# Optimization experiments

Hardware: AMD Instinct MI355X
Metric: run time of the kernel (lower is better)

The kernel has to match this reference:

```python
import jax, jax.numpy as jnp
import numpy as np

EPS = 1e-5
NEG_SLOPE = 0.01  # nn.LeakyReLU default


def _layer_norm(x, scale, bias):
    mu = jnp.mean(x, axis=-1, keepdims=True)
    var = jnp.mean(jnp.square(x - mu), axis=-1, keepdims=True)
    return (x - mu) * jax.lax.rsqrt(var + EPS) * scale + bias


def _graph_conv(x, W, b, edge_src, edge_dst, dinv_out, dinv_in, n_nodes):
    # DGL GraphConv, norm='both': rst = LeakyReLU( (D_in^{-1/2} A D_out^{-1/2} x) W + b )
    h = x * dinv_out[:, None]
    agg = jax.ops.segment_sum(h[edge_src], edge_dst, num_segments=n_nodes)
    rst = agg * dinv_in[:, None]
    return jax.nn.leaky_relu(rst @ W + b, NEG_SLOPE)


def setup_inputs() -> dict:
    key = jax.random.key(0)
    ks = jax.random.split(key, 12)
    B, NM, NE, NS, H = 128, 100, 50, 25, 768
    T = 256                      # node_type_embedding dim
    D = H + T                    # in_feat_dim = 1024
    OUT = 768                    # out_feat_dim
    L = 3                        # num_layers
    N_NODES = B * (NM + NE + NS) # 22400
    N_EDGES = 716800
    inp = {
        "mention_hidden_state": jax.random.normal(ks[0], (B, NM, H), jnp.float32),
        "entity_hidden_state": jax.random.normal(ks[1], (B, NE, H), jnp.float32),
        "sent_hidden_state": jax.random.normal(ks[2], (B, NS, H), jnp.float32),
        "edge_src": jax.random.randint(ks[3], (N_EDGES,), 0, N_NODES, jnp.int32),
        "edge_dst": jax.random.randint(ks[4], (N_EDGES,), 0, N_NODES, jnp.int32),
        "type_emb": jax.random.normal(ks[5], (3, T), jnp.float32),
        "ln_scale": jnp.ones((D,), jnp.float32),
        "ln_bias": jnp.zeros((D,), jnp.float32),
        "gcn_weights": jax.random.normal(ks[6], (L, D, D), jnp.float32) * (1.0 / np.sqrt(D)),
        "gcn_biases": jnp.zeros((L, D), jnp.float32),
        "fc_w": jax.random.normal(ks[7], (D, OUT), jnp.float32) * (1.0 / np.sqrt(D)),
        "fc_b": jnp.zeros((OUT,), jnp.float32),
    }
    return inp


def reference(mention_hidden_state, entity_hidden_state, sent_hidden_state,
              edge_src, edge_dst, type_emb, ln_scale, ln_bias,
              gcn_weights, gcn_biases, fc_w, fc_b):
    B, NM, H = mention_hidden_state.shape
    NE = entity_hidden_state.shape[1]
    NS = sent_hidden_state.shape[1]

    def add_type(x, t):
        te = jnp.broadcast_to(type_emb[t][None, None, :], (x.shape[0], x.shape[1], type_emb.shape[1]))
        return jnp.concatenate([x, te], axis=2)

    nodes = jnp.concatenate([
        add_type(mention_hidden_state, 0),
        add_type(entity_hidden_state, 1),
        add_type(sent_hidden_state, 2),
    ], axis=1)                                     # [B, N, D]
    nodes = _layer_norm(nodes, ln_scale, ln_bias)
    N = nodes.shape[1]
    D = nodes.shape[2]
    x = nodes.reshape(B * N, D)

    n_nodes = B * N
    ones = jnp.ones_like(edge_src, dtype=x.dtype)
    deg_out = jax.ops.segment_sum(ones, edge_src, num_segments=n_nodes)
    deg_in = jax.ops.segment_sum(ones, edge_dst, num_segments=n_nodes)
    dinv_out = jax.lax.rsqrt(jnp.clip(deg_out, 1.0))
    dinv_in = jax.lax.rsqrt(jnp.clip(deg_in, 1.0))

    for l in range(gcn_weights.shape[0]):
        x = _graph_conv(x, gcn_weights[l], gcn_biases[l], edge_src, edge_dst,
                        dinv_out, dinv_in, n_nodes)

    out = (x @ fc_w + fc_b).reshape(B, N, -1)
    return out[:, NM:NM + NE]                      # entity slice [B, NE, OUT]
```

## Files before the change

### kernel.cpp

```cpp
#include <hip/hip_runtime.h>
#include <cstdint>

using u16 = unsigned short;
using u32 = unsigned int;

typedef _Float16 h8 __attribute__((ext_vector_type(8)));
typedef _Float16 h4 __attribute__((ext_vector_type(4)));
typedef _Float16 h2 __attribute__((ext_vector_type(2)));
typedef float f32x4 __attribute__((ext_vector_type(4)));

#define N_PER_B 175
#define NN 22400
#define DCOL 1024

__device__ __forceinline__ void gload16(const void* g, void* l) {
  void* gnc = const_cast<void*>(g);
  __builtin_amdgcn_global_load_lds(
      (__attribute__((address_space(1))) unsigned int*)gnc,
      (__attribute__((address_space(3))) unsigned int*)l, 16, 0, 0);
}


__global__ void degree_k(const int* __restrict__ es, const int* __restrict__ ed,
                         u32* __restrict__ dout, u32* __restrict__ din, int nE) {
  int e = blockIdx.x * 256 + threadIdx.x;
  if (e < nE) {
    atomicAdd(&dout[es[e]], 1u);
    atomicAdd(&din[ed[e]], 1u);
  }
}

__global__ void dinv_k(const u32* __restrict__ dout, const u32* __restrict__ din,
                       float* __restrict__ vo, float* __restrict__ vi) {
  int i = blockIdx.x * 256 + threadIdx.x;
  if (i < NN) {
    u32 a = dout[i]; if (a == 0u) a = 1u;
    u32 b = din[i];  if (b == 0u) b = 1u;
    vo[i] = rsqrtf((float)a);
    vi[i] = rsqrtf((float)b);
  }
}

__global__ __launch_bounds__(1024) void scan_k(const u32* __restrict__ deg,
                                               u32* __restrict__ off, int n) {
  __shared__ u32 wsum[16];
  __shared__ u32 carry_s;
  int tid = threadIdx.x;
  int lane = tid & 63, w = tid >> 6;
  if (tid == 0) carry_s = 0u;
  __syncthreads();
  for (int base = 0; base < n; base += 1024) {
    u32 cb = carry_s;
    int i = base + tid;
    u32 v = (i < n) ? deg[i] : 0u;
    u32 x = v;
#pragma unroll
    for (int o = 1; o < 64; o <<= 1) {
      u32 t = __shfl_up(x, o);
      if (lane >= o) x += t;
    }
    if (lane == 63) wsum[w] = x;
    __syncthreads();
    u32 woff = 0;
#pragma unroll
    for (int j = 0; j < 16; ++j) { u32 s = wsum[j]; if (j < w) woff += s; }
    u32 incl = cb + woff + x;
    if (i < n) off[i] = incl - v;
    if (tid == 1023) carry_s = incl;
    __syncthreads();
  }
  if (tid == 0) off[n] = carry_s;
}

__global__ void scatter_k(const int* __restrict__ es, const int* __restrict__ ed,
                          const u32* __restrict__ off, u32* __restrict__ cur,
                          int* __restrict__ csr, int nE) {
  int e = blockIdx.x * 256 + threadIdx.x;
  if (e < nE) {
    int d = ed[e];
    u32 p = atomicAdd(&cur[d], 1u);
    csr[off[d] + p] = es[e];
  }
}


__global__ __launch_bounds__(256) void ln_k(const float* __restrict__ mh,
    const float* __restrict__ eh, const float* __restrict__ sh,
    const float* __restrict__ te, const float* __restrict__ sc,
    const float* __restrict__ bi, const float* __restrict__ dvo,
    _Float16* __restrict__ x0) {
  int node = blockIdx.x;
  int b = node / N_PER_B;
  int p = node - b * N_PER_B;
  const float* row;
  int t;
  if (p < 100)      { row = mh + ((size_t)b * 100 + p) * 768;        t = 0; }
  else if (p < 150) { row = eh + ((size_t)b * 50 + (p - 100)) * 768; t = 1; }
  else              { row = sh + ((size_t)b * 25 + (p - 150)) * 768; t = 2; }
  int tid = threadIdx.x;
  const float* lp = (tid < 192) ? (row + tid * 4) : (te + t * 256 + (tid - 192) * 4);
  float4 v = *(const float4*)lp;
  float s = v.x + v.y + v.z + v.w;
  float q = v.x * v.x + v.y * v.y + v.z * v.z + v.w * v.w;
#pragma unroll
  for (int o = 32; o > 0; o >>= 1) { s += __shfl_down(s, o); q += __shfl_down(q, o); }
  __shared__ float red[8];
  int w = tid >> 6;
  if ((tid & 63) == 0) { red[w] = s; red[4 + w] = q; }
  __syncthreads();
  float ts = red[0] + red[1] + red[2] + red[3];
  float tq = red[4] + red[5] + red[6] + red[7];
  float mu = ts * (1.0f / 1024.0f);
  float var = tq * (1.0f / 1024.0f) - mu * mu;
  float r = rsqrtf(var + 1e-5f);
  float scale_o = dvo[node];
  int c = tid * 4;
  float4 g  = *(const float4*)(sc + c);
  float4 hb = *(const float4*)(bi + c);
  h4 o;
  o.x = (_Float16)(((v.x - mu) * r * g.x + hb.x) * scale_o);
  o.y = (_Float16)(((v.y - mu) * r * g.y + hb.y) * scale_o);
  o.z = (_Float16)(((v.z - mu) * r * g.z + hb.z) * scale_o);
  o.w = (_Float16)(((v.w - mu) * r * g.w + hb.w) * scale_o);
  *(h4*)(x0 + (size_t)node * DCOL + c) = o;
}


__global__ __launch_bounds__(256) void transpose_k(const float* __restrict__ W,
    _Float16* __restrict__ Wt, int K, int N) {
  __shared__ float tile[32][33];
  int n0 = blockIdx.x * 32, k0 = blockIdx.y * 32;
  int tx = threadIdx.x & 31, ty = threadIdx.x >> 5;
#pragma unroll
  for (int i = 0; i < 32; i += 8)
    tile[ty + i][tx] = W[(size_t)(k0 + ty + i) * N + n0 + tx];
  __syncthreads();
#pragma unroll
  for (int i = 0; i < 32; i += 8)
    Wt[(size_t)(n0 + ty + i) * K + k0 + tx] = (_Float16)tile[tx][ty + i];
}


template<int ENT>
__global__ __launch_bounds__(256) void aggregate_k(const _Float16* __restrict__ xs,
    const u32* __restrict__ off, const int* __restrict__ srcs,
    const float* __restrict__ dvi, _Float16* __restrict__ out, int NG) {
  int wave = threadIdx.x >> 6;
  int lane = threadIdx.x & 63;
  int b = blockIdx.x;
  int chunk = b & 7;
  int grp = b >> 3;
  int blk = grp * 4 + wave;
  int d;
  if (ENT) { int bb = blk / 50; d = bb * N_PER_B + 100 + (blk - bb * 50); }
  else d = blk;
  u32 s0 = __builtin_amdgcn_readfirstlane(off[d]);
  u32 s1 = __builtin_amdgcn_readfirstlane(off[d + 1]);
  const h2* xc = (const h2*)xs + chunk * 64 + lane;
  h2 c0 = (h2)0.f, c1 = (h2)0.f, c2 = (h2)0.f, c3 = (h2)0.f;
  h2 c4 = (h2)0.f, c5 = (h2)0.f, c6 = (h2)0.f, c7 = (h2)0.f;
  h2 c8 = (h2)0.f, c9 = (h2)0.f, cA = (h2)0.f, cB = (h2)0.f;
  h2 cC = (h2)0.f, cD = (h2)0.f, cE = (h2)0.f, cF = (h2)0.f;
  for (u32 base = s0; base < s1; base += 64) {
    u32 nrem = s1 - base;
    u32 iters = nrem < 64u ? nrem : 64u;
    int sv = srcs[base + (lane < iters ? lane : 0u)];
    u32 j = 0;
    for (; j + 16 <= iters; j += 16) {
      int i0 = __builtin_amdgcn_readlane(sv, j + 0);
      int i1 = __builtin_amdgcn_readlane(sv, j + 1);
      int i2 = __builtin_amdgcn_readlane(sv, j + 2);
      int i3 = __builtin_amdgcn_readlane(sv, j + 3);
      int i4 = __builtin_amdgcn_readlane(sv, j + 4);
      int i5 = __builtin_amdgcn_readlane(sv, j + 5);
      int i6 = __builtin_amdgcn_readlane(sv, j + 6);
      int i7 = __builtin_amdgcn_readlane(sv, j + 7);
      int i8 = __builtin_amdgcn_readlane(sv, j + 8);
      int i9 = __builtin_amdgcn_readlane(sv, j + 9);
      int iA = __builtin_amdgcn_readlane(sv, j + 10);
      int iB = __builtin_amdgcn_readlane(sv, j + 11);
      int iC = __builtin_amdgcn_readlane(sv, j + 12);
      int iD = __builtin_amdgcn_readlane(sv, j + 13);
      int iE = __builtin_amdgcn_readlane(sv, j + 14);
      int iF = __builtin_amdgcn_readlane(sv, j + 15);
      h2 v0 = xc[(size_t)i0 * 512];
      h2 v1 = xc[(size_t)i1 * 512];
      h2 v2 = xc[(size_t)i2 * 512];
      h2 v3 = xc[(size_t)i3 * 512];
      h2 v4 = xc[(size_t)i4 * 512];
      h2 v5 = xc[(size_t)i5 * 512];
      h2 v6 = xc[(size_t)i6 * 512];
      h2 v7 = xc[(size_t)i7 * 512];
      h2 v8 = xc[(size_t)i8 * 512];
      h2 v9 = xc[(size_t)i9 * 512];
      h2 vA = xc[(size_t)iA * 512];
      h2 vB = xc[(size_t)iB * 512];
      h2 vC = xc[(size_t)iC * 512];
      h2 vD = xc[(size_t)iD * 512];
      h2 vE = xc[(size_t)iE * 512];
      h2 vF = xc[(size_t)iF * 512];
      c0 += v0; c1 += v1; c2 += v2; c3 += v3;
      c4 += v4; c5 += v5; c6 += v6; c7 += v7;
      c8 += v8; c9 += v9; cA += vA; cB += vB;
      cC += vC; cD += vD; cE += vE; cF += vF;
    }
    for (; j + 4 <= iters; j += 4) {
      int i0 = __builtin_amdgcn_readlane(sv, j + 0);
      int i1 = __builtin_amdgcn_readlane(sv, j + 1);
      int i2 = __builtin_amdgcn_readlane(sv, j + 2);
      int i3 = __builtin_amdgcn_readlane(sv, j + 3);
      h2 v0 = xc[(size_t)i0 * 512];
      h2 v1 = xc[(size_t)i1 * 512];
      h2 v2 = xc[(size_t)i2 * 512];
      h2 v3 = xc[(size_t)i3 * 512];
      c0 += v0; c1 += v1; c2 += v2; c3 += v3;
    }
    for (; j < iters; ++j) {
      int i0 = __builtin_amdgcn_readlane(sv, j);
      c0 += xc[(size_t)i0 * 512];
    }
  }
  c0 += c8; c1 += c9; c2 += cA; c3 += cB;
  c4 += cC; c5 += cD; c6 += cE; c7 += cF;
  float wi = dvi[d];
  float lo = (((float)c0.x + (float)c1.x) + ((float)c2.x + (float)c3.x)) +
             (((float)c4.x + (float)c5.x) + ((float)c6.x + (float)c7.x));
  float hi = (((float)c0.y + (float)c1.y) + ((float)c2.y + (float)c3.y)) +
             (((float)c4.y + (float)c5.y) + ((float)c6.y + (float)c7.y));
  h2 r;
  r.x = (_Float16)(lo * wi);
  r.y = (_Float16)(hi * wi);
  *((h2*)(out + (size_t)blk * DCOL) + chunk * 64 + lane) = r;
}


template<int EPI>
__global__ __launch_bounds__(256, 3) void gemm_bt(const _Float16* __restrict__ A,
    const _Float16* __restrict__ Bt, const float* __restrict__ bias,
    const float* __restrict__ dvo,
    _Float16* __restrict__ outh, float* __restrict__ outf, int N, int K) {
  __shared__ __align__(16) _Float16 sA[128 * 32];
  __shared__ __align__(16) _Float16 sB[128 * 32];
  int tid = threadIdx.x;
  int wave = tid >> 6, lane = tid & 63;
  int wm = wave & 1, wn = wave >> 1;
  int lane16 = lane & 15, quad = lane >> 4;
  int m0 = blockIdx.y * 128, n0 = blockIdx.x * 128;
  int srow  = lane >> 2;
  int scolb = (lane & 3) * 16;
  const char* aBase = (const char*)(A  + (size_t)(m0 + wave * 32 + srow) * K) + scolb;
  const char* bBase = (const char*)(Bt + (size_t)(n0 + wave * 32 + srow) * K) + scolb;
  const size_t rowSkip = (size_t)16 * K * sizeof(_Float16);
  _Float16* lA0 = &sA[(wave * 2 + 0) * 512];
  _Float16* lA1 = &sA[(wave * 2 + 1) * 512];
  _Float16* lB0 = &sB[(wave * 2 + 0) * 512];
  _Float16* lB1 = &sB[(wave * 2 + 1) * 512];

  f32x4 acc[4][4];
  f32x4 zero = {0.f, 0.f, 0.f, 0.f};
#pragma unroll
  for (int i = 0; i < 4; ++i)
#pragma unroll
    for (int j = 0; j < 4; ++j) acc[i][j] = zero;

  for (int k0 = 0; k0 < K; k0 += 32) {
    __syncthreads();
    size_t kb = (size_t)k0 * sizeof(_Float16);
    gload16(aBase + kb,           lA0);
    gload16(aBase + kb + rowSkip, lA1);
    gload16(bBase + kb,           lB0);
    gload16(bBase + kb + rowSkip, lB1);
    __syncthreads();
    h8 af[4], bq[4];
#pragma unroll
    for (int mt = 0; mt < 4; ++mt)
      af[mt] = *(const h8*)&sA[(wm * 64 + mt * 16 + lane16) * 32 + quad * 8];
#pragma unroll
    for (int nt = 0; nt < 4; ++nt)
      bq[nt] = *(const h8*)&sB[(wn * 64 + nt * 16 + lane16) * 32 + quad * 8];
#pragma unroll
    for (int mt = 0; mt < 4; ++mt)
#pragma unroll
      for (int nt = 0; nt < 4; ++nt)
        acc[mt][nt] = __builtin_amdgcn_mfma_f32_16x16x32_f16(af[mt], bq[nt], acc[mt][nt], 0, 0, 0);
  }

#pragma unroll
  for (int nt = 0; nt < 4; ++nt) {
    int n = n0 + wn * 64 + nt * 16 + lane16;
    float bv = bias[n];
#pragma unroll
    for (int mt = 0; mt < 4; ++mt) {
      int mb = m0 + wm * 64 + mt * 16 + quad * 4;
#pragma unroll
      for (int i = 0; i < 4; ++i) {
        float v = acc[mt][nt][i] + bv;
        if (EPI == 0) {
          v = (v > 0.f) ? v : 0.01f * v;
          v *= dvo[mb + i];
          outh[(size_t)(mb + i) * N + n] = (_Float16)v;
        } else if (EPI == 2) {
          v = (v > 0.f) ? v : 0.01f * v;
          outh[(size_t)(mb + i) * N + n] = (_Float16)v;
        } else {
          outf[(size_t)(mb + i) * N + n] = v;
        }
      }
    }
  }
}


extern "C" void kernel_launch(void* const* d_in, const int* in_sizes, int n_in,
                              void* d_out, int out_size, void* d_ws, size_t ws_size,
                              hipStream_t stream) {
  const float* mh  = (const float*)d_in[0];
  const float* eh  = (const float*)d_in[1];
  const float* sh  = (const float*)d_in[2];
  const int*   es  = (const int*)d_in[3];
  const int*   ed  = (const int*)d_in[4];
  const float* te  = (const float*)d_in[5];
  const float* lns = (const float*)d_in[6];
  const float* lnb = (const float*)d_in[7];
  const float* gw  = (const float*)d_in[8];
  const float* gb  = (const float*)d_in[9];
  const float* fw  = (const float*)d_in[10];
  const float* fb  = (const float*)d_in[11];
  float* out = (float*)d_out;
  int nE = in_sizes[3];

  char* p = (char*)d_ws;
  auto alloc = [&](size_t bytes) -> void* {
    void* r = (void*)p;
    p += (bytes + 255) & ~(size_t)255;
    return r;
  };
  _Float16* xbuf = (_Float16*)alloc((size_t)NN * DCOL * 2);
  _Float16* agg  = (_Float16*)alloc((size_t)NN * DCOL * 2);
  _Float16* wt   = (_Float16*)alloc((size_t)3 * 1024 * 1024 * 2);
  _Float16* wtfc = (_Float16*)alloc((size_t)768 * 1024 * 2);
  u32* deg_out = (u32*)alloc((size_t)NN * 4);
  u32* deg_in  = (u32*)alloc((size_t)NN * 4);
  u32* cursor  = (u32*)alloc((size_t)NN * 4);
  u32* csr_off = (u32*)alloc((size_t)(NN + 1) * 4);
  float* dvo = (float*)alloc((size_t)NN * 4);
  float* dvi = (float*)alloc((size_t)NN * 4);
  int* csr_src = (int*)alloc((size_t)nE * 4);

  hipMemsetAsync(deg_out, 0, (size_t)3 * NN * 4, stream);

  int eb = (nE + 255) / 256;
  degree_k<<<eb, 256, 0, stream>>>(es, ed, deg_out, deg_in, nE);
  dinv_k<<<(NN + 255) / 256, 256, 0, stream>>>(deg_out, deg_in, dvo, dvi);
  scan_k<<<1, 1024, 0, stream>>>(deg_in, csr_off, NN);
  scatter_k<<<eb, 256, 0, stream>>>(es, ed, csr_off, cursor, csr_src, nE);
  ln_k<<<NN, 256, 0, stream>>>(mh, eh, sh, te, lns, lnb, dvo, xbuf);
  transpose_k<<<dim3(32, 32), 256, 0, stream>>>(gw + 0 * 1048576, wt + 0 * 1048576, 1024, 1024);
  transpose_k<<<dim3(32, 32), 256, 0, stream>>>(gw + 1 * 1048576, wt + 1 * 1048576, 1024, 1024);
  transpose_k<<<dim3(32, 32), 256, 0, stream>>>(gw + 2 * 1048576, wt + 2 * 1048576, 1024, 1024);
  transpose_k<<<dim3(24, 32), 256, 0, stream>>>(fw, wtfc, 1024, 768);

  aggregate_k<0><<<8 * 5600, 256, 0, stream>>>(xbuf, csr_off, csr_src, dvi, agg, 5600);
  gemm_bt<0><<<dim3(8, 175), 256, 0, stream>>>(agg, wt + 0 * 1048576, gb + 0,    dvo, xbuf, nullptr, 1024, 1024);
  aggregate_k<0><<<8 * 5600, 256, 0, stream>>>(xbuf, csr_off, csr_src, dvi, agg, 5600);
  gemm_bt<0><<<dim3(8, 175), 256, 0, stream>>>(agg, wt + 1 * 1048576, gb + 1024, dvo, xbuf, nullptr, 1024, 1024);
  aggregate_k<1><<<8 * 1600, 256, 0, stream>>>(xbuf, csr_off, csr_src, dvi, agg, 1600);
  gemm_bt<2><<<dim3(8, 50), 256, 0, stream>>>(agg, wt + 2 * 1048576, gb + 2048, nullptr, xbuf, nullptr, 1024, 1024);
  gemm_bt<1><<<dim3(6, 50), 256, 0, stream>>>(xbuf, wtfc, fb, nullptr, nullptr, out, 768, 1024);
}
```

Before: 707.5 us.

## Split aggregation into two source-half passes and double GEMM K-slice per sync

Edges are bucketed per destination by whether the source lies in the first or second half of nodes. Aggregation runs as two kernel passes, each gathering only from half the feature matrix, to improve cache locality of the random gathers. The second pass reads back the fp16 partial and applies the in-degree scaling. Separately, the GEMM loads two 32-wide K panels per barrier pair, halving synchronizations at the cost of doubled LDS. The approach adds an extra partial-sum read/write and an fp16 intermediate rounding.

```diff
diff --git a/kernel.cpp b/kernel.cpp
--- a/kernel.cpp
+++ b/kernel.cpp
@@ -11,6 +11,7 @@
 
 #define N_PER_B 175
 #define NN 22400
+#define HALF_N 11200
 #define DCOL 1024
 
 __device__ __forceinline__ void gload16(const void* g, void* l) {
@@ -22,20 +23,21 @@
 
 
 __global__ void degree_k(const int* __restrict__ es, const int* __restrict__ ed,
-                         u32* __restrict__ dout, u32* __restrict__ din, int nE) {
+                         u32* __restrict__ dout, u32* __restrict__ din2, int nE) {
   int e = blockIdx.x * 256 + threadIdx.x;
   if (e < nE) {
-    atomicAdd(&dout[es[e]], 1u);
-    atomicAdd(&din[ed[e]], 1u);
-  }
-}
-
-__global__ void dinv_k(const u32* __restrict__ dout, const u32* __restrict__ din,
+    int s = es[e], d = ed[e];
+    atomicAdd(&dout[s], 1u);
+    atomicAdd(&din2[2 * d + (s >= HALF_N)], 1u);
+  }
+}
+
+__global__ void dinv_k(const u32* __restrict__ dout, const u32* __restrict__ din2,
                        float* __restrict__ vo, float* __restrict__ vi) {
   int i = blockIdx.x * 256 + threadIdx.x;
   if (i < NN) {
     u32 a = dout[i]; if (a == 0u) a = 1u;
-    u32 b = din[i];  if (b == 0u) b = 1u;
+    u32 b = din2[2 * i] + din2[2 * i + 1]; if (b == 0u) b = 1u;
     vo[i] = rsqrtf((float)a);
     vi[i] = rsqrtf((float)b);
   }
@@ -77,9 +79,10 @@
                           int* __restrict__ csr, int nE) {
   int e = blockIdx.x * 256 + threadIdx.x;
   if (e < nE) {
-    int d = ed[e];
-    u32 p = atomicAdd(&cur[d], 1u);
-    csr[off[d] + p] = es[e];
+    int s = es[e];
+    int seg = 2 * ed[e] + (s >= HALF_N);
+    u32 p = atomicAdd(&cur[seg], 1u);
+    csr[off[seg] + p] = s;
   }
 }
 
@@ -141,10 +144,10 @@
 }
 
 
-template<int ENT>
+template<int ENT, int PASS>
 __global__ __launch_bounds__(256) void aggregate_k(const _Float16* __restrict__ xs,
     const u32* __restrict__ off, const int* __restrict__ srcs,
-    const float* __restrict__ dvi, _Float16* __restrict__ out, int NG) {
+    const float* __restrict__ dvi, _Float16* __restrict__ agg, int NG) {
   int wave = threadIdx.x >> 6;
   int lane = threadIdx.x & 63;
   int b = blockIdx.x;
@@ -154,9 +157,13 @@
   int d;
   if (ENT) { int bb = blk / 50; d = bb * N_PER_B + 100 + (blk - bb * 50); }
   else d = blk;
-  u32 s0 = __builtin_amdgcn_readfirstlane(off[d]);
-  u32 s1 = __builtin_amdgcn_readfirstlane(off[d + 1]);
+  int seg = 2 * d + PASS;
+  u32 s0 = __builtin_amdgcn_readfirstlane(off[seg]);
+  u32 s1 = __builtin_amdgcn_readfirstlane(off[seg + 1]);
   const h2* xc = (const h2*)xs + chunk * 64 + lane;
+  h2* outp = (h2*)(agg + (size_t)blk * DCOL) + chunk * 64 + lane;
+  h2 part;
+  if (PASS) part = *outp;
   h2 c0 = (h2)0.f, c1 = (h2)0.f, c2 = (h2)0.f, c3 = (h2)0.f;
   h2 c4 = (h2)0.f, c5 = (h2)0.f, c6 = (h2)0.f, c7 = (h2)0.f;
   h2 c8 = (h2)0.f, c9 = (h2)0.f, cA = (h2)0.f, cB = (h2)0.f;
@@ -222,15 +229,20 @@
   }
   c0 += c8; c1 += c9; c2 += cA; c3 += cB;
   c4 += cC; c5 += cD; c6 += cE; c7 += cF;
-  float wi = dvi[d];
   float lo = (((float)c0.x + (float)c1.x) + ((float)c2.x + (float)c3.x)) +
              (((float)c4.x + (float)c5.x) + ((float)c6.x + (float)c7.x));
   float hi = (((float)c0.y + (float)c1.y) + ((float)c2.y + (float)c3.y)) +
              (((float)c4.y + (float)c5.y) + ((float)c6.y + (float)c7.y));
   h2 r;
-  r.x = (_Float16)(lo * wi);
-  r.y = (_Float16)(hi * wi);
-  *((h2*)(out + (size_t)blk * DCOL) + chunk * 64 + lane) = r;
+  if (PASS == 0) {
+    r.x = (_Float16)lo;
+    r.y = (_Float16)hi;
+  } else {
+    float wi = dvi[d];
+    r.x = (_Float16)((lo + (float)part.x) * wi);
+    r.y = (_Float16)((hi + (float)part.y) * wi);
+  }
+  *outp = r;
 }
 
 
@@ -239,8 +251,8 @@
     const _Float16* __restrict__ Bt, const float* __restrict__ bias,
     const float* __restrict__ dvo,
     _Float16* __restrict__ outh, float* __restrict__ outf, int N, int K) {
-  __shared__ __align__(16) _Float16 sA[128 * 32];
-  __shared__ __align__(16) _Float16 sB[128 * 32];
+  __shared__ __align__(16) _Float16 sA[2][128 * 32];
+  __shared__ __align__(16) _Float16 sB[2][128 * 32];
   int tid = threadIdx.x;
   int wave = tid >> 6, lane = tid & 63;
   int wm = wave & 1, wn = wave >> 1;
@@ -251,10 +263,14 @@
   const char* aBase = (const char*)(A  + (size_t)(m0 + wave * 32 + srow) * K) + scolb;
   const char* bBase = (const char*)(Bt + (size_t)(n0 + wave * 32 + srow) * K) + scolb;
   const size_t rowSkip = (size_t)16 * K * sizeof(_Float16);
-  _Float16* lA0 = &sA[(wave * 2 + 0) * 512];
-  _Float16* lA1 = &sA[(wave * 2 + 1) * 512];
-  _Float16* lB0 = &sB[(wave * 2 + 0) * 512];
-  _Float16* lB1 = &sB[(wave * 2 + 1) * 512];
+  _Float16* lA0 = &sA[0][(wave * 2 + 0) * 512];
+  _Float16* lA1 = &sA[0][(wave * 2 + 1) * 512];
+  _Float16* lB0 = &sB[0][(wave * 2 + 0) * 512];
+  _Float16* lB1 = &sB[0][(wave * 2 + 1) * 512];
+  _Float16* lA0b = &sA[1][(wave * 2 + 0) * 512];
+  _Float16* lA1b = &sA[1][(wave * 2 + 1) * 512];
+  _Float16* lB0b = &sB[1][(wave * 2 + 0) * 512];
+  _Float16* lB1b = &sB[1][(wave * 2 + 1) * 512];
 
   f32x4 acc[4][4];
   f32x4 zero = {0.f, 0.f, 0.f, 0.f};
@@ -263,26 +279,33 @@
 #pragma unroll
     for (int j = 0; j < 4; ++j) acc[i][j] = zero;
 
-  for (int k0 = 0; k0 < K; k0 += 32) {
+  for (int k0 = 0; k0 < K; k0 += 64) {
     __syncthreads();
     size_t kb = (size_t)k0 * sizeof(_Float16);
-    gload16(aBase + kb,           lA0);
-    gload16(aBase + kb + rowSkip, lA1);
-    gload16(bBase + kb,           lB0);
-    gload16(bBase + kb + rowSkip, lB1);
+    gload16(aBase + kb,                lA0);
+    gload16(aBase + kb + rowSkip,      lA1);
+    gload16(bBase + kb,                lB0);
+    gload16(bBase + kb + rowSkip,      lB1);
+    gload16(aBase + kb + 64,           lA0b);
+    gload16(aBase + kb + 64 + rowSkip, lA1b);
+    gload16(bBase + kb + 64,           lB0b);
+    gload16(bBase + kb + 64 + rowSkip, lB1b);
     __syncthreads();
-    h8 af[4], bq[4];
-#pragma unroll
-    for (int mt = 0; mt < 4; ++mt)
-      af[mt] = *(const h8*)&sA[(wm * 64 + mt * 16 + lane16) * 32 + quad * 8];
-#pragma unroll
-    for (int nt = 0; nt < 4; ++nt)
-      bq[nt] = *(const h8*)&sB[(wn * 64 + nt * 16 + lane16) * 32 + quad * 8];
-#pragma unroll
-    for (int mt = 0; mt < 4; ++mt)
+#pragma unroll
+    for (int pnl = 0; pnl < 2; ++pnl) {
+      h8 af[4], bq[4];
+#pragma unroll
+      for (int mt = 0; mt < 4; ++mt)
+        af[mt] = *(const h8*)&sA[pnl][(wm * 64 + mt * 16 + lane16) * 32 + quad * 8];
 #pragma unroll
       for (int nt = 0; nt < 4; ++nt)
-        acc[mt][nt] = __builtin_amdgcn_mfma_f32_16x16x32_f16(af[mt], bq[nt], acc[mt][nt], 0, 0, 0);
+        bq[nt] = *(const h8*)&sB[pnl][(wn * 64 + nt * 16 + lane16) * 32 + quad * 8];
+#pragma unroll
+      for (int mt = 0; mt < 4; ++mt)
+#pragma unroll
+        for (int nt = 0; nt < 4; ++nt)
+          acc[mt][nt] = __builtin_amdgcn_mfma_f32_16x16x32_f16(af[mt], bq[nt], acc[mt][nt], 0, 0, 0);
+    }
   }
 
 #pragma unroll
@@ -340,19 +363,19 @@
   _Float16* wt   = (_Float16*)alloc((size_t)3 * 1024 * 1024 * 2);
   _Float16* wtfc = (_Float16*)alloc((size_t)768 * 1024 * 2);
   u32* deg_out = (u32*)alloc((size_t)NN * 4);
-  u32* deg_in  = (u32*)alloc((size_t)NN * 4);
-  u32* cursor  = (u32*)alloc((size_t)NN * 4);
-  u32* csr_off = (u32*)alloc((size_t)(NN + 1) * 4);
+  u32* din2    = (u32*)alloc((size_t)2 * NN * 4);
+  u32* cursor  = (u32*)alloc((size_t)2 * NN * 4);
+  u32* csr_off = (u32*)alloc((size_t)(2 * NN + 1) * 4);
   float* dvo = (float*)alloc((size_t)NN * 4);
   float* dvi = (float*)alloc((size_t)NN * 4);
   int* csr_src = (int*)alloc((size_t)nE * 4);
 
-  hipMemsetAsync(deg_out, 0, (size_t)3 * NN * 4, stream);
+  hipMemsetAsync(deg_out, 0, (size_t)5 * NN * 4, stream);
 
   int eb = (nE + 255) / 256;
-  degree_k<<<eb, 256, 0, stream>>>(es, ed, deg_out, deg_in, nE);
-  dinv_k<<<(NN + 255) / 256, 256, 0, stream>>>(deg_out, deg_in, dvo, dvi);
-  scan_k<<<1, 1024, 0, stream>>>(deg_in, csr_off, NN);
+  degree_k<<<eb, 256, 0, stream>>>(es, ed, deg_out, din2, nE);
+  dinv_k<<<(NN + 255) / 256, 256, 0, stream>>>(deg_out, din2, dvo, dvi);
+  scan_k<<<1, 1024, 0, stream>>>(din2, csr_off, 2 * NN);
   scatter_k<<<eb, 256, 0, stream>>>(es, ed, csr_off, cursor, csr_src, nE);
   ln_k<<<NN, 256, 0, stream>>>(mh, eh, sh, te, lns, lnb, dvo, xbuf);
   transpose_k<<<dim3(32, 32), 256, 0, stream>>>(gw + 0 * 1048576, wt + 0 * 1048576, 1024, 1024);
@@ -360,11 +383,14 @@
   transpose_k<<<dim3(32, 32), 256, 0, stream>>>(gw + 2 * 1048576, wt + 2 * 1048576, 1024, 1024);
   transpose_k<<<dim3(24, 32), 256, 0, stream>>>(fw, wtfc, 1024, 768);
 
-  aggregate_k<0><<<8 * 5600, 256, 0, stream>>>(xbuf, csr_off, csr_src, dvi, agg, 5600);
+  aggregate_k<0, 0><<<8 * 5600, 256, 0, stream>>>(xbuf, csr_off, csr_src, dvi, agg, 5600);
+  aggregate_k<0, 1><<<8 * 5600, 256, 0, stream>>>(xbuf, csr_off, csr_src, dvi, agg, 5600);
   gemm_bt<0><<<dim3(8, 175), 256, 0, stream>>>(agg, wt + 0 * 1048576, gb + 0,    dvo, xbuf, nullptr, 1024, 1024);
-  aggregate_k<0><<<8 * 5600, 256, 0, stream>>>(xbuf, csr_off, csr_src, dvi, agg, 5600);
+  aggregate_k<0, 0><<<8 * 5600, 256, 0, stream>>>(xbuf, csr_off, csr_src, dvi, agg, 5600);
+  aggregate_k<0, 1><<<8 * 5600, 256, 0, stream>>>(xbuf, csr_off, csr_src, dvi, agg, 5600);
   gemm_bt<0><<<dim3(8, 175), 256, 0, stream>>>(agg, wt + 1 * 1048576, gb + 1024, dvo, xbuf, nullptr, 1024, 1024);
-  aggregate_k<1><<<8 * 1600, 256, 0, stream>>>(xbuf, csr_off, csr_src, dvi, agg, 1600);
+  aggregate_k<1, 0><<<8 * 1600, 256, 0, stream>>>(xbuf, csr_off, csr_src, dvi, agg, 1600);
+  aggregate_k<1, 1><<<8 * 1600, 256, 0, stream>>>(xbuf, csr_off, csr_src, dvi, agg, 1600);
   gemm_bt<2><<<dim3(8, 50), 256, 0, stream>>>(agg, wt + 2 * 1048576, gb + 2048, nullptr, xbuf, nullptr, 1024, 1024);
   gemm_bt<1><<<dim3(6, 50), 256, 0, stream>>>(xbuf, wtfc, fb, nullptr, nullptr, out, 768, 1024);
 }
```

Result: slower. 792.5 us (+12.0%).

## Remap GEMM blocks per XCD and double K-step per barrier pair

Applied to the files above, without the earlier changes.

The GEMM now uses a 1D grid and remaps block ids so that each of the 8 XCDs works on a contiguous range of M tiles. This is meant to improve L2 reuse of the A rows, since the A tiles stay local to one XCD's cache. It also loads two 32-wide K panels per iteration, halving the number of syncthreads barriers per K. The cost is doubled LDS use, which may lower occupancy, and some padded blocks exit early.

```diff
diff --git a/kernel.cpp b/kernel.cpp
--- a/kernel.cpp
+++ b/kernel.cpp
@@ -238,23 +238,37 @@
 __global__ __launch_bounds__(256, 3) void gemm_bt(const _Float16* __restrict__ A,
     const _Float16* __restrict__ Bt, const float* __restrict__ bias,
     const float* __restrict__ dvo,
-    _Float16* __restrict__ outh, float* __restrict__ outf, int N, int K) {
-  __shared__ __align__(16) _Float16 sA[128 * 32];
-  __shared__ __align__(16) _Float16 sB[128 * 32];
+    _Float16* __restrict__ outh, float* __restrict__ outf,
+    int N, int K, int Mtiles, int NBN) {
+  int id = blockIdx.x;
+  int xcd = id & 7;
+  int rest = id >> 3;
+  int ntile = rest % NBN;
+  int mloc = rest / NBN;
+  int mpx = (Mtiles + 7) >> 3;
+  int mtile = xcd * mpx + mloc;
+  if (mtile >= Mtiles) return;
+  int m0 = mtile * 128, n0 = ntile * 128;
+
+  __shared__ __align__(16) _Float16 sA[2][128 * 32];
+  __shared__ __align__(16) _Float16 sB[2][128 * 32];
   int tid = threadIdx.x;
   int wave = tid >> 6, lane = tid & 63;
   int wm = wave & 1, wn = wave >> 1;
   int lane16 = lane & 15, quad = lane >> 4;
-  int m0 = blockIdx.y * 128, n0 = blockIdx.x * 128;
   int srow  = lane >> 2;
   int scolb = (lane & 3) * 16;
   const char* aBase = (const char*)(A  + (size_t)(m0 + wave * 32 + srow) * K) + scolb;
   const char* bBase = (const char*)(Bt + (size_t)(n0 + wave * 32 + srow) * K) + scolb;
   const size_t rowSkip = (size_t)16 * K * sizeof(_Float16);
-  _Float16* lA0 = &sA[(wave * 2 + 0) * 512];
-  _Float16* lA1 = &sA[(wave * 2 + 1) * 512];
-  _Float16* lB0 = &sB[(wave * 2 + 0) * 512];
-  _Float16* lB1 = &sB[(wave * 2 + 1) * 512];
+  _Float16* lA0 = &sA[0][(wave * 2 + 0) * 512];
+  _Float16* lA1 = &sA[0][(wave * 2 + 1) * 512];
+  _Float16* lB0 = &sB[0][(wave * 2 + 0) * 512];
+  _Float16* lB1 = &sB[0][(wave * 2 + 1) * 512];
+  _Float16* lA0b = &sA[1][(wave * 2 + 0) * 512];
+  _Float16* lA1b = &sA[1][(wave * 2 + 1) * 512];
+  _Float16* lB0b = &sB[1][(wave * 2 + 0) * 512];
+  _Float16* lB1b = &sB[1][(wave * 2 + 1) * 512];
 
   f32x4 acc[4][4];
   f32x4 zero = {0.f, 0.f, 0.f, 0.f};
@@ -263,26 +277,33 @@
 #pragma unroll
     for (int j = 0; j < 4; ++j) acc[i][j] = zero;
 
-  for (int k0 = 0; k0 < K; k0 += 32) {
+  for (int k0 = 0; k0 < K; k0 += 64) {
     __syncthreads();
     size_t kb = (size_t)k0 * sizeof(_Float16);
-    gload16(aBase + kb,           lA0);
-    gload16(aBase + kb + rowSkip, lA1);
-    gload16(bBase + kb,           lB0);
-    gload16(bBase + kb + rowSkip, lB1);
+    gload16(aBase + kb,                lA0);
+    gload16(aBase + kb + rowSkip,      lA1);
+    gload16(bBase + kb,                lB0);
+    gload16(bBase + kb + rowSkip,      lB1);
+    gload16(aBase + kb + 64,           lA0b);
+    gload16(aBase + kb + 64 + rowSkip, lA1b);
+    gload16(bBase + kb + 64,           lB0b);
+    gload16(bBase + kb + 64 + rowSkip, lB1b);
     __syncthreads();
-    h8 af[4], bq[4];
-#pragma unroll
-    for (int mt = 0; mt < 4; ++mt)
-      af[mt] = *(const h8*)&sA[(wm * 64 + mt * 16 + lane16) * 32 + quad * 8];
-#pragma unroll
-    for (int nt = 0; nt < 4; ++nt)
-      bq[nt] = *(const h8*)&sB[(wn * 64 + nt * 16 + lane16) * 32 + quad * 8];
-#pragma unroll
-    for (int mt = 0; mt < 4; ++mt)
+#pragma unroll
+    for (int pnl = 0; pnl < 2; ++pnl) {
+      h8 af[4], bq[4];
+#pragma unroll
+      for (int mt = 0; mt < 4; ++mt)
+        af[mt] = *(const h8*)&sA[pnl][(wm * 64 + mt * 16 + lane16) * 32 + quad * 8];
 #pragma unroll
       for (int nt = 0; nt < 4; ++nt)
-        acc[mt][nt] = __builtin_amdgcn_mfma_f32_16x16x32_f16(af[mt], bq[nt], acc[mt][nt], 0, 0, 0);
+        bq[nt] = *(const h8*)&sB[pnl][(wn * 64 + nt * 16 + lane16) * 32 + quad * 8];
+#pragma unroll
+      for (int mt = 0; mt < 4; ++mt)
+#pragma unroll
+        for (int nt = 0; nt < 4; ++nt)
+          acc[mt][nt] = __builtin_amdgcn_mfma_f32_16x16x32_f16(af[mt], bq[nt], acc[mt][nt], 0, 0, 0);
+    }
   }
 
 #pragma unroll
@@ -360,11 +381,12 @@
   transpose_k<<<dim3(32, 32), 256, 0, stream>>>(gw + 2 * 1048576, wt + 2 * 1048576, 1024, 1024);
   transpose_k<<<dim3(24, 32), 256, 0, stream>>>(fw, wtfc, 1024, 768);
 
+
   aggregate_k<0><<<8 * 5600, 256, 0, stream>>>(xbuf, csr_off, csr_src, dvi, agg, 5600);
-  gemm_bt<0><<<dim3(8, 175), 256, 0, stream>>>(agg, wt + 0 * 1048576, gb + 0,    dvo, xbuf, nullptr, 1024, 1024);
+  gemm_bt<0><<<1408, 256, 0, stream>>>(agg, wt + 0 * 1048576, gb + 0,    dvo, xbuf, nullptr, 1024, 1024, 175, 8);
   aggregate_k<0><<<8 * 5600, 256, 0, stream>>>(xbuf, csr_off, csr_src, dvi, agg, 5600);
-  gemm_bt<0><<<dim3(8, 175), 256, 0, stream>>>(agg, wt + 1 * 1048576, gb + 1024, dvo, xbuf, nullptr, 1024, 1024);
+  gemm_bt<0><<<1408, 256, 0, stream>>>(agg, wt + 1 * 1048576, gb + 1024, dvo, xbuf, nullptr, 1024, 1024, 175, 8);
   aggregate_k<1><<<8 * 1600, 256, 0, stream>>>(xbuf, csr_off, csr_src, dvi, agg, 1600);
-  gemm_bt<2><<<dim3(8, 50), 256, 0, stream>>>(agg, wt + 2 * 1048576, gb + 2048, nullptr, xbuf, nullptr, 1024, 1024);
-  gemm_bt<1><<<dim3(6, 50), 256, 0, stream>>>(xbuf, wtfc, fb, nullptr, nullptr, out, 768, 1024);
-}
+  gemm_bt<2><<<448, 256, 0, stream>>>(agg, wt + 2 * 1048576, gb + 2048, nullptr, xbuf, nullptr, 1024, 1024, 50, 8);
+  gemm_bt<1><<<336, 256, 0, stream>>>(xbuf, wtfc, fb, nullptr, nullptr, out, 768, 1024, 50, 6);
+}
```

Result: faster. 664.6 us (-6.1%).
